# Optimization experiments

Measured on AMD Instinct MI355X. Metric: run time of the kernel, lower is better.

Reference implementation:

```python
import jax, jax.numpy as jnp
import numpy as np

NUM_HEADS = 8
HIDDEN_DIM = 64
N_REAL = 30000
N_VIRT = 2000
N_NODES = N_REAL + N_VIRT
N_EDGES = 512000
VOCAB = 100000


def setup_inputs() -> dict:
    key = jax.random.key(0)
    k1, k2, k3, k4, k5 = jax.random.split(key, 5)
    features = jax.random.normal(k1, (VOCAB, HIDDEN_DIM), dtype=jnp.float32)
    virtue_emb = jax.random.normal(k2, (N_VIRT, HIDDEN_DIM), dtype=jnp.float32)  # nn.Embedding weight ~ N(0,1)
    cnodes = jax.random.randint(k3, (N_REAL,), 0, VOCAB, dtype=jnp.int64)
    src = jax.random.randint(k4, (N_EDGES,), 0, N_NODES, dtype=jnp.int64)
    dst = jax.random.randint(k5, (N_EDGES,), 0, N_NODES, dtype=jnp.int64)
    vm_idx = jnp.arange(N_VIRT, dtype=jnp.int64) + N_REAL  # virtual nodes are appended after real nodes
    return {"features": features, "virtue_emb": virtue_emb, "cnodes": cnodes,
            "src": src, "dst": dst, "vm_idx": vm_idx}


def _edge_softmax(e, dst, n_nodes):
    # DGL edge_softmax: softmax over incoming edges of each destination node.
    m = jax.ops.segment_max(e, dst, num_segments=n_nodes)          # [N,H,1]
    ex = jnp.exp(e - m[dst])                                       # [E,H,1]
    s = jax.ops.segment_sum(ex, dst, num_segments=n_nodes)        # [N,H,1]
    return ex / s[dst]


def reference(features, virtue_emb, cnodes, src, dst, vm_idx):
    real_ndata = features[cnodes]                                  # [R,D] F.embedding
    ndata = jnp.concatenate([real_ndata, virtue_emb], axis=0)      # [N,D]
    n = ndata.shape[0]
    # agg_type='neighbor': cat([h]*H, dim=1).view(-1,H,D) == broadcast along head dim
    nft = jnp.broadcast_to(ndata[:, None, :], (n, NUM_HEADS, HIDDEN_DIM))
    e = jnp.ones((src.shape[0], NUM_HEADS, 1), dtype=ndata.dtype)
    eft = _edge_softmax(e, dst, n)                                 # [E,H,1]
    new_nft = jax.ops.segment_sum(nft[src] * eft, dst, num_segments=n)      # round 1: u_mul_e / sum
    final_nft = jax.ops.segment_sum(new_nft[src] * eft, dst, num_segments=n)  # round 2
    return final_nft[vm_idx]                                       # [V,H,D]
```

## Files before the change

kernel.cpp:

```cpp
#include <hip/hip_runtime.h>

constexpr int HEADS  = 8;
constexpr int DIM    = 64;
constexpr int NREAL  = 30000;
constexpr int NVIRT  = 2000;
constexpr int NNODES = NREAL + NVIRT;
constexpr int NEDGES = 512000;
constexpr int STRIDE = 64;

typedef _Float16 half4 __attribute__((ext_vector_type(4)));


__global__ __launch_bounds__(256) void k_prep(const float* __restrict__ features,
                                              const float* __restrict__ virtue,
                                              const int* __restrict__ cnodes,
                                              const int* __restrict__ src,
                                              const int* __restrict__ dst,
                                              _Float16* __restrict__ ndata,
                                              int* __restrict__ cnt,
                                              unsigned char* __restrict__ mark,
                                              unsigned short* __restrict__ slots) {
  int i = blockIdx.x * blockDim.x + threadIdx.x;
  {
    int node = i >> 4;
    int q    = i & 15;
    const float4* srcp = (node < NREAL)
        ? (const float4*)(features + (long)cnodes[node] * DIM)
        : (const float4*)(virtue + (long)(node - NREAL) * DIM);
    float4 v = srcp[q];
    half4 h = { (_Float16)v.x, (_Float16)v.y, (_Float16)v.z, (_Float16)v.w };
    ((half4*)(ndata + (long)node * DIM))[q] = h;
  }
  {
    int d = dst[i];
    int s = src[i];
    int pos = atomicAdd(&cnt[d], 1);
    if (pos < STRIDE) slots[(long)d * STRIDE + pos] = (unsigned short)s;
    if (d >= NREAL) mark[s] = 1;
  }
}

__global__ __launch_bounds__(256) void k_agg1(const int* __restrict__ cnt,
                                              const unsigned char* __restrict__ mark,
                                              const unsigned short* __restrict__ slots,
                                              const _Float16* __restrict__ ndata,
                                              float* __restrict__ new_nft) {
  int node = blockIdx.x * 4 + (threadIdx.x >> 6);
  if (node >= NNODES) return;
  if (!mark[node]) return;
  int lane = threadIdx.x & 63;
  int q = lane >> 4;
  int l = lane & 15;
  int deg = cnt[node];
  if (deg > STRIDE) deg = STRIDE;
  int myidx = 0;
  if (lane < deg) myidx = (int)slots[(long)node * STRIDE + lane];
  float4 acc  = make_float4(0.f, 0.f, 0.f, 0.f);
  float4 acc2 = make_float4(0.f, 0.f, 0.f, 0.f);
  const half4* nd = (const half4*)ndata;
  for (int k0 = 0; k0 < deg; k0 += 8) {
    int ka = k0 + q;
    int kb = k0 + q + 4;
    int sa = __shfl(myidx, ka);
    int sb = __shfl(myidx, kb);
    if (ka < deg) {
      half4 v = nd[(long)sa * 16 + l];
      acc.x += (float)v.x; acc.y += (float)v.y; acc.z += (float)v.z; acc.w += (float)v.w;
    }
    if (kb < deg) {
      half4 v = nd[(long)sb * 16 + l];
      acc2.x += (float)v.x; acc2.y += (float)v.y; acc2.z += (float)v.z; acc2.w += (float)v.w;
    }
  }
  acc.x += acc2.x; acc.y += acc2.y; acc.z += acc2.z; acc.w += acc2.w;
  acc.x += __shfl_xor(acc.x, 16); acc.y += __shfl_xor(acc.y, 16);
  acc.z += __shfl_xor(acc.z, 16); acc.w += __shfl_xor(acc.w, 16);
  acc.x += __shfl_xor(acc.x, 32); acc.y += __shfl_xor(acc.y, 32);
  acc.z += __shfl_xor(acc.z, 32); acc.w += __shfl_xor(acc.w, 32);
  if (q == 0) {
    float inv = (deg > 0) ? 1.0f / (float)deg : 0.0f;
    acc.x *= inv; acc.y *= inv; acc.z *= inv; acc.w *= inv;
    ((float4*)new_nft)[(long)node * 16 + l] = acc;
  }
}

__global__ __launch_bounds__(256) void k_agg2(const int* __restrict__ cnt,
                                              const unsigned short* __restrict__ slots,
                                              const float* __restrict__ new_nft,
                                              float* __restrict__ out) {
  int v = blockIdx.x * 4 + (threadIdx.x >> 6);
  if (v >= NVIRT) return;
  int node = NREAL + v;
  int lane = threadIdx.x & 63;
  int q = lane >> 4;
  int l = lane & 15;
  int deg = cnt[node];
  if (deg > STRIDE) deg = STRIDE;
  int myidx = 0;
  if (lane < deg) myidx = (int)slots[(long)node * STRIDE + lane];
  float4 acc  = make_float4(0.f, 0.f, 0.f, 0.f);
  float4 acc2 = make_float4(0.f, 0.f, 0.f, 0.f);
  const float4* nf4 = (const float4*)new_nft;
  for (int k0 = 0; k0 < deg; k0 += 8) {
    int ka = k0 + q;
    int kb = k0 + q + 4;
    int sa = __shfl(myidx, ka);
    int sb = __shfl(myidx, kb);
    if (ka < deg) {
      float4 x = nf4[(long)sa * 16 + l];
      acc.x += x.x; acc.y += x.y; acc.z += x.z; acc.w += x.w;
    }
    if (kb < deg) {
      float4 x = nf4[(long)sb * 16 + l];
      acc2.x += x.x; acc2.y += x.y; acc2.z += x.z; acc2.w += x.w;
    }
  }
  acc.x += acc2.x; acc.y += acc2.y; acc.z += acc2.z; acc.w += acc2.w;
  acc.x += __shfl_xor(acc.x, 16); acc.y += __shfl_xor(acc.y, 16);
  acc.z += __shfl_xor(acc.z, 16); acc.w += __shfl_xor(acc.w, 16);
  acc.x += __shfl_xor(acc.x, 32); acc.y += __shfl_xor(acc.y, 32);
  acc.z += __shfl_xor(acc.z, 32); acc.w += __shfl_xor(acc.w, 32);
  if (q == 0) {
    float inv = (deg > 0) ? 1.0f / (float)deg : 0.0f;
    acc.x *= inv; acc.y *= inv; acc.z *= inv; acc.w *= inv;
    float4* o4 = (float4*)out;
#pragma unroll
    for (int h = 0; h < HEADS; ++h)
      o4[((long)v * HEADS + h) * 16 + l] = acc;
  }
}


extern "C" void kernel_launch(void* const* d_in, const int* in_sizes, int n_in,
                              void* d_out, int out_size, void* d_ws, size_t ws_size,
                              hipStream_t stream) {
  const float* features = (const float*)d_in[0];
  const float* virtue   = (const float*)d_in[1];
  const int*   cnodes   = (const int*)d_in[2];
  const int*   src      = (const int*)d_in[3];
  const int*   dst      = (const int*)d_in[4];
  float* out = (float*)d_out;

  float*          new_nft = (float*)d_ws;
  _Float16*       ndata   = (_Float16*)(new_nft + (long)NNODES * DIM);
  int*            cnt     = (int*)(ndata + (long)NNODES * DIM);
  unsigned char*  mark    = (unsigned char*)(cnt + NNODES);
  unsigned short* slots   = (unsigned short*)(mark + NNODES);

  const int B = 256;

  hipMemsetAsync(cnt, 0, NNODES * sizeof(int) + NNODES, stream);
  k_prep<<<NEDGES / B, B, 0, stream>>>(features, virtue, cnodes, src, dst,
                                       ndata, cnt, mark, slots);
  k_agg1<<<(NNODES + 3) / 4, B, 0, stream>>>(cnt, mark, slots, ndata, new_nft);
  k_agg2<<<(NVIRT + 3) / 4, B, 0, stream>>>(cnt, slots, new_nft, out);
}
```

Before: 128.6 us.

## Fuse prep and both aggregation rounds into one cooperative kernel with worklist

Replaces the memset and three separate kernel launches with a single cooperative kernel that uses grid-wide syncs between the zeroing, prep, round-1 and round-2 phases. Round 1 now iterates over a compact worklist of marked nodes, built with atomicExch and atomicAdd, instead of launching a wave for every node and exiting early. This removes launch gaps and idle waves. In exchange it adds grid.sync overhead, extra atomics during prep, and a fixed 1024-block grid that must be fully co-resident.

```diff
diff --git a/kernel.cpp b/kernel.cpp
--- a/kernel.cpp
+++ b/kernel.cpp
@@ -1,4 +1,7 @@
 #include <hip/hip_runtime.h>
+#include <hip/hip_cooperative_groups.h>
+
+namespace cg = cooperative_groups;
 
 constexpr int HEADS  = 8;
 constexpr int DIM    = 64;
@@ -8,125 +11,138 @@
 constexpr int NEDGES = 512000;
 constexpr int STRIDE = 64;
 
+constexpr int NBLK  = 1024;
+constexpr int NTHR  = 256;
+constexpr int NTOT  = NBLK * NTHR;
+constexpr int NWAVE = NTOT / 64;
+
 typedef _Float16 half4 __attribute__((ext_vector_type(4)));
 
+__global__ __launch_bounds__(NTHR, 4) void k_fused(
+    const float* __restrict__ features,
+    const float* __restrict__ virtue,
+    const int* __restrict__ cnodes,
+    const int* __restrict__ src,
+    const int* __restrict__ dst,
+    _Float16* __restrict__ ndata,
+    float* __restrict__ new_nft,
+    int* __restrict__ cnt,
+    int* __restrict__ mark,
+    int* __restrict__ nmarked,
+    int* __restrict__ wl,
+    unsigned short* __restrict__ slots,
+    float* __restrict__ out)
+{
+  cg::grid_group grid = cg::this_grid();
+  const int t = blockIdx.x * NTHR + threadIdx.x;
 
-__global__ __launch_bounds__(256) void k_prep(const float* __restrict__ features,
-                                              const float* __restrict__ virtue,
-                                              const int* __restrict__ cnodes,
-                                              const int* __restrict__ src,
-                                              const int* __restrict__ dst,
-                                              _Float16* __restrict__ ndata,
-                                              int* __restrict__ cnt,
-                                              unsigned char* __restrict__ mark,
-                                              unsigned short* __restrict__ slots) {
-  int i = blockIdx.x * blockDim.x + threadIdx.x;
-  {
-    int node = i >> 4;
-    int q    = i & 15;
-    const float4* srcp = (node < NREAL)
-        ? (const float4*)(features + (long)cnodes[node] * DIM)
-        : (const float4*)(virtue + (long)(node - NREAL) * DIM);
-    float4 v = srcp[q];
-    half4 h = { (_Float16)v.x, (_Float16)v.y, (_Float16)v.z, (_Float16)v.w };
-    ((half4*)(ndata + (long)node * DIM))[q] = h;
-  }
-  {
-    int d = dst[i];
-    int s = src[i];
-    int pos = atomicAdd(&cnt[d], 1);
-    if (pos < STRIDE) slots[(long)d * STRIDE + pos] = (unsigned short)s;
-    if (d >= NREAL) mark[s] = 1;
-  }
-}
+  if (t < 16001) ((int4*)cnt)[t] = make_int4(0, 0, 0, 0);
+  grid.sync();
 
-__global__ __launch_bounds__(256) void k_agg1(const int* __restrict__ cnt,
-                                              const unsigned char* __restrict__ mark,
-                                              const unsigned short* __restrict__ slots,
-                                              const _Float16* __restrict__ ndata,
-                                              float* __restrict__ new_nft) {
-  int node = blockIdx.x * 4 + (threadIdx.x >> 6);
-  if (node >= NNODES) return;
-  if (!mark[node]) return;
-  int lane = threadIdx.x & 63;
-  int q = lane >> 4;
-  int l = lane & 15;
-  int deg = cnt[node];
-  if (deg > STRIDE) deg = STRIDE;
-  int myidx = 0;
-  if (lane < deg) myidx = (int)slots[(long)node * STRIDE + lane];
-  float4 acc  = make_float4(0.f, 0.f, 0.f, 0.f);
-  float4 acc2 = make_float4(0.f, 0.f, 0.f, 0.f);
-  const half4* nd = (const half4*)ndata;
-  for (int k0 = 0; k0 < deg; k0 += 8) {
-    int ka = k0 + q;
-    int kb = k0 + q + 4;
-    int sa = __shfl(myidx, ka);
-    int sb = __shfl(myidx, kb);
-    if (ka < deg) {
-      half4 v = nd[(long)sa * 16 + l];
-      acc.x += (float)v.x; acc.y += (float)v.y; acc.z += (float)v.z; acc.w += (float)v.w;
+  for (int i = t; i < NEDGES; i += NTOT) {
+    {
+      int node = i >> 4;
+      int q16  = i & 15;
+      const float4* srcp = (node < NREAL)
+          ? (const float4*)(features + (long)cnodes[node] * DIM)
+          : (const float4*)(virtue + (long)(node - NREAL) * DIM);
+      float4 v = srcp[q16];
+      half4 h = { (_Float16)v.x, (_Float16)v.y, (_Float16)v.z, (_Float16)v.w };
+      ((half4*)(ndata + (long)node * DIM))[q16] = h;
     }
-    if (kb < deg) {
-      half4 v = nd[(long)sb * 16 + l];
-      acc2.x += (float)v.x; acc2.y += (float)v.y; acc2.z += (float)v.z; acc2.w += (float)v.w;
+    {
+      int d = dst[i];
+      int s = src[i];
+      int pos = atomicAdd(&cnt[d], 1);
+      if (pos < STRIDE) slots[(long)d * STRIDE + pos] = (unsigned short)s;
+      if (d >= NREAL) {
+        if (atomicExch(&mark[s], 1) == 0) {
+          int p = atomicAdd(nmarked, 1);
+          wl[p] = s;
+        }
+      }
     }
   }
-  acc.x += acc2.x; acc.y += acc2.y; acc.z += acc2.z; acc.w += acc2.w;
-  acc.x += __shfl_xor(acc.x, 16); acc.y += __shfl_xor(acc.y, 16);
-  acc.z += __shfl_xor(acc.z, 16); acc.w += __shfl_xor(acc.w, 16);
-  acc.x += __shfl_xor(acc.x, 32); acc.y += __shfl_xor(acc.y, 32);
-  acc.z += __shfl_xor(acc.z, 32); acc.w += __shfl_xor(acc.w, 32);
-  if (q == 0) {
-    float inv = (deg > 0) ? 1.0f / (float)deg : 0.0f;
-    acc.x *= inv; acc.y *= inv; acc.z *= inv; acc.w *= inv;
-    ((float4*)new_nft)[(long)node * 16 + l] = acc;
-  }
-}
+  grid.sync();
 
-__global__ __launch_bounds__(256) void k_agg2(const int* __restrict__ cnt,
-                                              const unsigned short* __restrict__ slots,
-                                              const float* __restrict__ new_nft,
-                                              float* __restrict__ out) {
-  int v = blockIdx.x * 4 + (threadIdx.x >> 6);
-  if (v >= NVIRT) return;
-  int node = NREAL + v;
-  int lane = threadIdx.x & 63;
-  int q = lane >> 4;
-  int l = lane & 15;
-  int deg = cnt[node];
-  if (deg > STRIDE) deg = STRIDE;
-  int myidx = 0;
-  if (lane < deg) myidx = (int)slots[(long)node * STRIDE + lane];
-  float4 acc  = make_float4(0.f, 0.f, 0.f, 0.f);
-  float4 acc2 = make_float4(0.f, 0.f, 0.f, 0.f);
-  const float4* nf4 = (const float4*)new_nft;
-  for (int k0 = 0; k0 < deg; k0 += 8) {
-    int ka = k0 + q;
-    int kb = k0 + q + 4;
-    int sa = __shfl(myidx, ka);
-    int sb = __shfl(myidx, kb);
-    if (ka < deg) {
-      float4 x = nf4[(long)sa * 16 + l];
-      acc.x += x.x; acc.y += x.y; acc.z += x.z; acc.w += x.w;
+  const int wid  = t >> 6;
+  const int lane = t & 63;
+  const int q    = lane >> 4;
+  const int l    = lane & 15;
+  const int M    = *nmarked;
+  const half4* nd = (const half4*)ndata;
+
+  for (int w = wid; w < M; w += NWAVE) {
+    int node = wl[w];
+    int deg = cnt[node];
+    if (deg > STRIDE) deg = STRIDE;
+    int myidx = 0;
+    if (lane < deg) myidx = (int)slots[(long)node * STRIDE + lane];
+    float4 acc  = make_float4(0.f, 0.f, 0.f, 0.f);
+    float4 acc2 = make_float4(0.f, 0.f, 0.f, 0.f);
+    for (int k0 = 0; k0 < deg; k0 += 8) {
+      int ka = k0 + q;
+      int kb = k0 + q + 4;
+      int sa = __shfl(myidx, ka);
+      int sb = __shfl(myidx, kb);
+      if (ka < deg) {
+        half4 v = nd[(long)sa * 16 + l];
+        acc.x += (float)v.x; acc.y += (float)v.y; acc.z += (float)v.z; acc.w += (float)v.w;
+      }
+      if (kb < deg) {
+        half4 v = nd[(long)sb * 16 + l];
+        acc2.x += (float)v.x; acc2.y += (float)v.y; acc2.z += (float)v.z; acc2.w += (float)v.w;
+      }
     }
-    if (kb < deg) {
-      float4 x = nf4[(long)sb * 16 + l];
-      acc2.x += x.x; acc2.y += x.y; acc2.z += x.z; acc2.w += x.w;
+    acc.x += acc2.x; acc.y += acc2.y; acc.z += acc2.z; acc.w += acc2.w;
+    acc.x += __shfl_xor(acc.x, 16); acc.y += __shfl_xor(acc.y, 16);
+    acc.z += __shfl_xor(acc.z, 16); acc.w += __shfl_xor(acc.w, 16);
+    acc.x += __shfl_xor(acc.x, 32); acc.y += __shfl_xor(acc.y, 32);
+    acc.z += __shfl_xor(acc.z, 32); acc.w += __shfl_xor(acc.w, 32);
+    if (q == 0) {
+      float inv = (deg > 0) ? 1.0f / (float)deg : 0.0f;
+      acc.x *= inv; acc.y *= inv; acc.z *= inv; acc.w *= inv;
+      ((float4*)new_nft)[(long)node * 16 + l] = acc;
     }
   }
-  acc.x += acc2.x; acc.y += acc2.y; acc.z += acc2.z; acc.w += acc2.w;
-  acc.x += __shfl_xor(acc.x, 16); acc.y += __shfl_xor(acc.y, 16);
-  acc.z += __shfl_xor(acc.z, 16); acc.w += __shfl_xor(acc.w, 16);
-  acc.x += __shfl_xor(acc.x, 32); acc.y += __shfl_xor(acc.y, 32);
-  acc.z += __shfl_xor(acc.z, 32); acc.w += __shfl_xor(acc.w, 32);
-  if (q == 0) {
-    float inv = (deg > 0) ? 1.0f / (float)deg : 0.0f;
-    acc.x *= inv; acc.y *= inv; acc.z *= inv; acc.w *= inv;
-    float4* o4 = (float4*)out;
+  grid.sync();
+
+  const float4* nf4 = (const float4*)new_nft;
+  for (int v = wid; v < NVIRT; v += NWAVE) {
+    int node = NREAL + v;
+    int deg = cnt[node];
+    if (deg > STRIDE) deg = STRIDE;
+    int myidx = 0;
+    if (lane < deg) myidx = (int)slots[(long)node * STRIDE + lane];
+    float4 acc  = make_float4(0.f, 0.f, 0.f, 0.f);
+    float4 acc2 = make_float4(0.f, 0.f, 0.f, 0.f);
+    for (int k0 = 0; k0 < deg; k0 += 8) {
+      int ka = k0 + q;
+      int kb = k0 + q + 4;
+      int sa = __shfl(myidx, ka);
+      int sb = __shfl(myidx, kb);
+      if (ka < deg) {
+        float4 x = nf4[(long)sa * 16 + l];
+        acc.x += x.x; acc.y += x.y; acc.z += x.z; acc.w += x.w;
+      }
+      if (kb < deg) {
+        float4 x = nf4[(long)sb * 16 + l];
+        acc2.x += x.x; acc2.y += x.y; acc2.z += x.z; acc2.w += x.w;
+      }
+    }
+    acc.x += acc2.x; acc.y += acc2.y; acc.z += acc2.z; acc.w += acc2.w;
+    acc.x += __shfl_xor(acc.x, 16); acc.y += __shfl_xor(acc.y, 16);
+    acc.z += __shfl_xor(acc.z, 16); acc.w += __shfl_xor(acc.w, 16);
+    acc.x += __shfl_xor(acc.x, 32); acc.y += __shfl_xor(acc.y, 32);
+    acc.z += __shfl_xor(acc.z, 32); acc.w += __shfl_xor(acc.w, 32);
+    if (q == 0) {
+      float inv = (deg > 0) ? 1.0f / (float)deg : 0.0f;
+      acc.x *= inv; acc.y *= inv; acc.z *= inv; acc.w *= inv;
+      float4* o4 = (float4*)out;
 #pragma unroll
-    for (int h = 0; h < HEADS; ++h)
-      o4[((long)v * HEADS + h) * 16 + l] = acc;
+      for (int h = 0; h < HEADS; ++h)
+        o4[((long)v * HEADS + h) * 16 + l] = acc;
+    }
   }
 }
 
@@ -143,15 +159,17 @@
 
   float*          new_nft = (float*)d_ws;
   _Float16*       ndata   = (_Float16*)(new_nft + (long)NNODES * DIM);
-  int*            cnt     = (int*)(ndata + (long)NNODES * DIM);
-  unsigned char*  mark    = (unsigned char*)(cnt + NNODES);
-  unsigned short* slots   = (unsigned short*)(mark + NNODES);
+  unsigned short* slots   = (unsigned short*)(ndata + (long)NNODES * DIM);
+  int*            cnt     = (int*)(slots + (long)NNODES * STRIDE);
+  int*            mark    = cnt + NNODES;
+  int*            nmarked = mark + NNODES;
+  int*            wl      = nmarked + 4;
 
-  const int B = 256;
-
-  hipMemsetAsync(cnt, 0, NNODES * sizeof(int) + NNODES, stream);
-  k_prep<<<NEDGES / B, B, 0, stream>>>(features, virtue, cnodes, src, dst,
-                                       ndata, cnt, mark, slots);
-  k_agg1<<<(NNODES + 3) / 4, B, 0, stream>>>(cnt, mark, slots, ndata, new_nft);
-  k_agg2<<<(NVIRT + 3) / 4, B, 0, stream>>>(cnt, slots, new_nft, out);
+  void* args[] = {
+    (void*)&features, (void*)&virtue, (void*)&cnodes, (void*)&src, (void*)&dst,
+    (void*)&ndata, (void*)&new_nft, (void*)&cnt, (void*)&mark,
+    (void*)&nmarked, (void*)&wl, (void*)&slots, (void*)&out
+  };
+  hipLaunchCooperativeKernel((const void*)k_fused, dim3(NBLK), dim3(NTHR),
+                             args, 0, stream);
 }
```

Measured after the change: 457.8 us. 256% more time.
